# Kernel optimization log

Measured on AMD Instinct MI355X. Metric: run time of the kernel, lower is better.

## Reference

```python
import jax, jax.numpy as jnp
import numpy as np

B, T, D_IN, D_MODEL = 4, 4096, 256, 128


def setup_inputs() -> dict:
    key = jax.random.key(0)
    ks = jax.random.split(key, 7)
    s_in = 1.0 / np.sqrt(D_IN)
    return {
        "x": jax.random.normal(ks[0], (B, T, D_IN), dtype=jnp.float32),
        "Wq": jax.random.normal(ks[1], (D_IN, D_MODEL), dtype=jnp.float32) * s_in,
        "bq": jnp.zeros((D_MODEL,), dtype=jnp.float32),
        "Wk": jax.random.normal(ks[2], (D_IN, D_MODEL), dtype=jnp.float32) * s_in,
        "bk": jnp.zeros((D_MODEL,), dtype=jnp.float32),
        "Wv": jax.random.normal(ks[3], (D_IN, D_MODEL), dtype=jnp.float32) * s_in,
        "bv": jnp.zeros((D_MODEL,), dtype=jnp.float32),
    }


def reference(x, Wq, bq, Wk, bk, Wv, bv):
    # projections: (B,T,d_in) @ (d_in,d_model) -> (B,T,d_model)
    q = x @ Wq + bq
    k = x @ Wk + bk
    v = x @ Wv + bv
    # scores: (B,T,T), scaled by sqrt(d_model)
    scores = jnp.einsum("btd,bsd->bts", q, k) / np.sqrt(D_MODEL).astype(np.float32)
    attn = jax.nn.softmax(scores, axis=-1)
    out = jnp.einsum("bts,bsd->btd", attn, v)
    return out, attn
```

## Files before the change

kernel.cpp:

```cpp
#include <hip/hip_runtime.h>
#include <hip/hip_bf16.h>
#include <stdint.h>

#define TT 4096
#define DM 128
#define DIN 256
#define NB 4

typedef __attribute__((ext_vector_type(4))) float f32x4;
typedef __attribute__((ext_vector_type(8))) short s16x8;
typedef __attribute__((ext_vector_type(4))) short s16x4;

__device__ __forceinline__ unsigned short f2bf(float f) {
    union { float f; unsigned int u; } v; v.f = f;
    return (unsigned short)((v.u + 0x7FFFu + ((v.u >> 16) & 1u)) >> 16);
}
__device__ __forceinline__ float bf2f(unsigned short h) {
    union { unsigned int u; float f; } v; v.u = ((unsigned int)h) << 16;
    return v.f;
}

__global__ __launch_bounds__(256) void k_wt(const float* __restrict__ Wq,
                                            const float* __restrict__ Wk,
                                            const float* __restrict__ Wv,
                                            unsigned short* __restrict__ Wtb) {
    int tid = blockIdx.x * 256 + threadIdx.x;
    int m = tid >> 15;
    int r = tid & 32767;
    int n = r >> 8;
    int k = r & 255;
    const float* W = (m == 0) ? Wq : (m == 1) ? Wk : Wv;
    Wtb[(size_t)tid] = f2bf(W[k * DM + n]);
}

__global__ __launch_bounds__(256) void k_proj(const float* __restrict__ x,
        const float* __restrict__ bq, const float* __restrict__ bk, const float* __restrict__ bv,
        const unsigned short* __restrict__ Wtb,
        unsigned short* __restrict__ Qb, unsigned short* __restrict__ Kb,
        unsigned short* __restrict__ Vb) {
    __shared__ __align__(16) unsigned short wt[DM][40];
    __shared__ __align__(16) unsigned short xl[64][40];
    int m = blockIdx.x >> 8;
    int tile = blockIdx.x & 255;
    int rowbase = tile * 64;
    int i = threadIdx.x;
    int w = i >> 6, l = i & 63;
    int lg = l >> 4, ll = l & 15;
    const float* bias = (m == 0) ? bq : (m == 1) ? bk : bv;
    unsigned short* out = (m == 0) ? Qb : (m == 1) ? Kb : Vb;
    const unsigned short* wsrc = Wtb + (size_t)m * DM * DIN;

    f32x4 acc[8];
    for (int n = 0; n < 8; n++) acc[n] = (f32x4){0.f, 0.f, 0.f, 0.f};

    for (int kk = 0; kk < 8; kk++) {
        int k0 = kk * 32;
        for (int t = 0; t < 2; t++) {
            int idx = i + t * 256;
            int row = idx >> 2, c8 = idx & 3;
            s16x8 v = *(const s16x8*)(wsrc + (size_t)row * DIN + k0 + c8 * 8);
            *(s16x8*)(&wt[row][c8 * 8]) = v;
        }
        for (int t = 0; t < 2; t++) {
            int idx = i + t * 256;
            int row = idx >> 3, c4 = idx & 7;
            f32x4 v = *(const f32x4*)(x + (size_t)(rowbase + row) * DIN + k0 + c4 * 4);
            s16x4 h;
            for (int j = 0; j < 4; j++) h[j] = (short)f2bf(v[j]);
            *(s16x4*)(&xl[row][c4 * 4]) = h;
        }
        __syncthreads();
        s16x8 a = *(const s16x8*)(&xl[w * 16 + ll][lg * 8]);
        for (int n = 0; n < 8; n++) {
            s16x8 b = *(const s16x8*)(&wt[n * 16 + ll][lg * 8]);
            acc[n] = __builtin_amdgcn_mfma_f32_16x16x32_bf16(a, b, acc[n], 0, 0, 0);
        }
        __syncthreads();
    }
    for (int n = 0; n < 8; n++) {
        int col = n * 16 + ll;
        float bv_ = bias[col];
        for (int j = 0; j < 4; j++) {
            int row = rowbase + w * 16 + lg * 4 + j;
            out[(size_t)row * DM + col] = f2bf(acc[n][j] + bv_);
        }
    }
}

__global__ __launch_bounds__(256) void k_vt(const unsigned short* __restrict__ Vb,
                                            unsigned short* __restrict__ Vtb) {
    __shared__ __align__(16) unsigned short tile[64][72];
    int bid = blockIdx.x;
    int b = bid >> 7;
    int rem = bid & 127;
    int tI = rem >> 1, dI = rem & 1;
    int t0 = tI * 64, d0 = dI * 64;
    int i = threadIdx.x;
    for (int t = 0; t < 2; t++) {
        int idx = i + t * 256;
        int r = idx >> 3, c8 = idx & 7;
        s16x8 v = *(const s16x8*)(Vb + ((size_t)(b * TT) + t0 + r) * DM + d0 + c8 * 8);
        *(s16x8*)(&tile[r][c8 * 8]) = v;
    }
    __syncthreads();
    for (int t = 0; t < 2; t++) {
        int idx = i + t * 256;
        int r2 = idx >> 3, c8 = idx & 7;
        s16x8 v;
        for (int j = 0; j < 8; j++) v[j] = (short)tile[c8 * 8 + j][r2];
        *(s16x8*)(Vtb + ((size_t)b * DM + d0 + r2) * TT + t0 + c8 * 8) = v;
    }
}

__global__ __launch_bounds__(512) void k_attn(const unsigned short* __restrict__ Qb,
        const unsigned short* __restrict__ Kb, const unsigned short* __restrict__ Vtb,
        float* __restrict__ outO, float* __restrict__ outA) {
    __shared__ __align__(16) char smem[40448];
    unsigned short* Kl = (unsigned short*)smem;
    unsigned short* Vl = (unsigned short*)(smem + 17408);
    unsigned short* Pl = (unsigned short*)(smem + 35840);

    int bid = blockIdx.x;
    int id2 = (bid & 7) * 64 + (bid >> 3);
    int b = id2 >> 7;
    int rowbase = (id2 & 127) * 32;
    int i = threadIdx.x;
    int w = i >> 6, l = i & 63;
    int rh = w & 1, kh = w >> 1;
    int r2 = w & 1, h2 = (w >> 1) & 1, c2 = w >> 2;
    int lg = l >> 4, ll = l & 15;

    const unsigned short* Qrow = Qb + ((size_t)(b * TT) + rowbase) * DM;
    const unsigned short* Krow = Kb + (size_t)(b * TT) * DM;
    const unsigned short* Vtb_b = Vtb + (size_t)b * DM * TT;
    const float scale = 0.08838834764831845f;

    s16x8 qf[4];
    for (int c = 0; c < 4; c++)
        qf[c] = *(const s16x8*)(Qrow + (size_t)(rh * 16 + ll) * DM + c * 32 + lg * 8);

    float rs[4] = {0.f, 0.f, 0.f, 0.f};
    for (int s0 = 0; s0 < TT; s0 += 64) {
        for (int t = 0; t < 2; t++) {
            int idx = i + t * 512;
            int row = idx >> 4, c8 = idx & 15;
            s16x8 v = *(const s16x8*)(Krow + (size_t)(s0 + row) * DM + c8 * 8);
            *(s16x8*)(&Kl[row * 136 + c8 * 8]) = v;
        }
        __syncthreads();
        {
            f32x4 acc = (f32x4){0.f, 0.f, 0.f, 0.f};
            int kcol = kh * 16 + ll;
            for (int c = 0; c < 4; c++) {
                s16x8 bfr = *(const s16x8*)(&Kl[kcol * 136 + c * 32 + lg * 8]);
                acc = __builtin_amdgcn_mfma_f32_16x16x32_bf16(qf[c], bfr, acc, 0, 0, 0);
            }
            for (int j = 0; j < 4; j++) rs[j] += __expf(acc[j] * scale);
        }
        __syncthreads();
    }
    for (int mm = 1; mm < 16; mm <<= 1)
        for (int j = 0; j < 4; j++) rs[j] += __shfl_xor(rs[j], mm, 64);
    float* rsx = (float*)Pl;
    if (ll == 0)
        for (int j = 0; j < 4; j++) rsx[(kh * 2 + rh) * 16 + lg * 4 + j] = rs[j];
    __syncthreads();
    float inv[4];
    for (int j = 0; j < 4; j++) {
        float tot = rsx[(0 * 2 + rh) * 16 + lg * 4 + j] + rsx[(1 * 2 + rh) * 16 + lg * 4 + j]
                  + rsx[(2 * 2 + rh) * 16 + lg * 4 + j] + rsx[(3 * 2 + rh) * 16 + lg * 4 + j];
        inv[j] = 1.0f / tot;
    }

    f32x4 oacc[4];
    for (int n = 0; n < 4; n++) oacc[n] = (f32x4){0.f, 0.f, 0.f, 0.f};

    for (int s0 = 0; s0 < TT; s0 += 64) {
        for (int t = 0; t < 2; t++) {
            int idx = i + t * 512;
            int row = idx >> 4, c8 = idx & 15;
            s16x8 v = *(const s16x8*)(Krow + (size_t)(s0 + row) * DM + c8 * 8);
            *(s16x8*)(&Kl[row * 136 + c8 * 8]) = v;
        }
        for (int t = 0; t < 2; t++) {
            int idx = i + t * 512;
            int row = idx >> 3, c8 = idx & 7;
            s16x8 v = *(const s16x8*)(Vtb_b + (size_t)row * TT + s0 + c8 * 8);
            *(s16x8*)(&Vl[row * 72 + c8 * 8]) = v;
        }
        __syncthreads();
        {
            f32x4 acc = (f32x4){0.f, 0.f, 0.f, 0.f};
            int kcol = kh * 16 + ll;
            for (int c = 0; c < 4; c++) {
                s16x8 bfr = *(const s16x8*)(&Kl[kcol * 136 + c * 32 + lg * 8]);
                acc = __builtin_amdgcn_mfma_f32_16x16x32_bf16(qf[c], bfr, acc, 0, 0, 0);
            }
            for (int j = 0; j < 4; j++) {
                float p = __expf(acc[j] * scale) * inv[j];
                outA[((size_t)(b * TT) + rowbase + rh * 16 + lg * 4 + j) * TT
                     + s0 + kh * 16 + ll] = p;
                Pl[(rh * 16 + lg * 4 + j) * 72 + kh * 16 + ll] = f2bf(p);
            }
        }
        __syncthreads();
        {
            s16x8 af = *(const s16x8*)(&Pl[(r2 * 16 + ll) * 72 + h2 * 32 + lg * 8]);
            for (int n8 = 0; n8 < 4; n8++) {
                s16x8 bfr = *(const s16x8*)(&Vl[(c2 * 64 + n8 * 16 + ll) * 72 + h2 * 32 + lg * 8]);
                oacc[n8] = __builtin_amdgcn_mfma_f32_16x16x32_bf16(af, bfr, oacc[n8], 0, 0, 0);
            }
        }
        __syncthreads();
    }

    float* Osc = (float*)smem;
    if (h2 == 0) {
        for (int n8 = 0; n8 < 4; n8++)
            for (int j = 0; j < 4; j++) {
                int row = r2 * 16 + lg * 4 + j, col = c2 * 64 + n8 * 16 + ll;
                Osc[row * 132 + col] = oacc[n8][j];
            }
    }
    __syncthreads();
    if (h2 == 1) {
        for (int n8 = 0; n8 < 4; n8++)
            for (int j = 0; j < 4; j++) {
                int row = r2 * 16 + lg * 4 + j, col = c2 * 64 + n8 * 16 + ll;
                float v = oacc[n8][j] + Osc[row * 132 + col];
                outO[((size_t)(b * TT) + rowbase + row) * DM + col] = v;
            }
    }
}

extern "C" void kernel_launch(void* const* d_in, const int* in_sizes, int n_in,
                              void* d_out, int out_size, void* d_ws, size_t ws_size,
                              hipStream_t stream) {
    const float* x  = (const float*)d_in[0];
    const float* Wq = (const float*)d_in[1];
    const float* bq = (const float*)d_in[2];
    const float* Wk = (const float*)d_in[3];
    const float* bk = (const float*)d_in[4];
    const float* Wv = (const float*)d_in[5];
    const float* bv = (const float*)d_in[6];
    float* outO = (float*)d_out;
    float* outA = outO + (size_t)NB * TT * DM;

    char* ws = (char*)d_ws;
    unsigned short* Qb  = (unsigned short*)(ws);
    unsigned short* Kb  = (unsigned short*)(ws + ((size_t)1 << 22));
    unsigned short* Vb  = (unsigned short*)(ws + ((size_t)2 << 22));
    unsigned short* Vtb = (unsigned short*)(ws + ((size_t)3 << 22));
    unsigned short* Wtb = (unsigned short*)(ws + ((size_t)4 << 22));

    k_wt<<<dim3(384), dim3(256), 0, stream>>>(Wq, Wk, Wv, Wtb);
    k_proj<<<dim3(768), dim3(256), 0, stream>>>(x, bq, bk, bv, Wtb, Qb, Kb, Vb);
    k_vt<<<dim3(512), dim3(256), 0, stream>>>(Vb, Vtb);
    k_attn<<<dim3(512), dim3(512), 0, stream>>>(Qb, Kb, Vtb, outO, outA);
}
```

Before: 160.6 us.

## Pipeline K/V tiles into LDS with async direct-to-LDS loads and XOR swizzle

Replaces the synchronous register-staged K and V tile loads in both attention passes with global_load_lds direct-to-LDS copies. The row-sum pass uses a triple-buffered K tile and the output pass a double-buffered K/V tile, so loads for future tiles run while the current tile's MFMAs execute. Synchronisation moves from __syncthreads to explicit vmcnt/lgkmcnt waits plus s_barrier. An XOR swizzle on the source addresses replaces padded LDS rows to avoid bank conflicts. This raises LDS use to about 70 KB per block, which may lower occupancy. The vmcnt counts also depend on the interleaved outA stores being counted in order.

Result: faster. 132.8 us (-17.4%).

```diff
diff --git a/kernel.cpp b/kernel.cpp
--- a/kernel.cpp
+++ b/kernel.cpp
@@ -15,9 +15,11 @@
     union { float f; unsigned int u; } v; v.f = f;
     return (unsigned short)((v.u + 0x7FFFu + ((v.u >> 16) & 1u)) >> 16);
 }
-__device__ __forceinline__ float bf2f(unsigned short h) {
-    union { unsigned int u; float f; } v; v.u = ((unsigned int)h) << 16;
-    return v.f;
+
+__device__ __forceinline__ void cp16(const void* g, void* l) {
+    __builtin_amdgcn_global_load_lds(
+        (__attribute__((address_space(1))) unsigned int*)(size_t)g,
+        (__attribute__((address_space(3))) unsigned int*)l, 16, 0, 0);
 }
 
 __global__ __launch_bounds__(256) void k_wt(const float* __restrict__ Wq,
@@ -115,10 +117,8 @@
 __global__ __launch_bounds__(512) void k_attn(const unsigned short* __restrict__ Qb,
         const unsigned short* __restrict__ Kb, const unsigned short* __restrict__ Vtb,
         float* __restrict__ outO, float* __restrict__ outA) {
-    __shared__ __align__(16) char smem[40448];
-    unsigned short* Kl = (unsigned short*)smem;
-    unsigned short* Vl = (unsigned short*)(smem + 17408);
-    unsigned short* Pl = (unsigned short*)(smem + 35840);
+    __shared__ __align__(16) char smem[70144];
+    unsigned short* Pl = (unsigned short*)(smem + 65536);
 
     int bid = blockIdx.x;
     int id2 = (bid & 7) * 64 + (bid >> 3);
@@ -135,29 +135,57 @@
     const unsigned short* Vtb_b = Vtb + (size_t)b * DM * TT;
     const float scale = 0.08838834764831845f;
 
+    int kch0 = w * 2;
+    int krow_l = l >> 4;
+    int kg_l = l & 15;
+    int vch0 = w * 2;
+    int vrow_l = l >> 3;
+    int vg_l = l & 7;
+
     s16x8 qf[4];
     for (int c = 0; c < 4; c++)
         qf[c] = *(const s16x8*)(Qrow + (size_t)(rh * 16 + ll) * DM + c * 32 + lg * 8);
 
+    int kr = kh * 16 + ll;
+
     float rs[4] = {0.f, 0.f, 0.f, 0.f};
-    for (int s0 = 0; s0 < TT; s0 += 64) {
-        for (int t = 0; t < 2; t++) {
-            int idx = i + t * 512;
-            int row = idx >> 4, c8 = idx & 15;
-            s16x8 v = *(const s16x8*)(Krow + (size_t)(s0 + row) * DM + c8 * 8);
-            *(s16x8*)(&Kl[row * 136 + c8 * 8]) = v;
-        }
-        __syncthreads();
-        {
+    {
+        for (int pt = 0; pt < 2; pt++) {
+            char* kbuf = smem + pt * 16384;
+            for (int t = 0; t < 2; t++) {
+                int ch = kch0 + t;
+                int row = pt * 64 + ch * 4 + krow_l;
+                int g = kg_l ^ (row & 7);
+                cp16(Krow + (size_t)row * DM + g * 8, kbuf + ch * 1024);
+            }
+        }
+        asm volatile("s_waitcnt vmcnt(2)" ::: "memory");
+        __builtin_amdgcn_s_barrier();
+
+        int idx = 0;
+        for (int t = 0; t < 64; t++) {
+            if (t + 2 < 64) {
+                int pidx = idx + 2; if (pidx >= 3) pidx -= 3;
+                char* kbuf = smem + pidx * 16384;
+                int s0n = (t + 2) * 64;
+                for (int u = 0; u < 2; u++) {
+                    int ch = kch0 + u;
+                    int row = ch * 4 + krow_l;
+                    int g = kg_l ^ (row & 7);
+                    cp16(Krow + (size_t)(s0n + row) * DM + g * 8, kbuf + ch * 1024);
+                }
+            }
+            const char* kb = smem + idx * 16384 + kr * 256;
             f32x4 acc = (f32x4){0.f, 0.f, 0.f, 0.f};
-            int kcol = kh * 16 + ll;
             for (int c = 0; c < 4; c++) {
-                s16x8 bfr = *(const s16x8*)(&Kl[kcol * 136 + c * 32 + lg * 8]);
+                s16x8 bfr = *(const s16x8*)(kb + (((c * 4 + lg) ^ (kr & 7)) << 4));
                 acc = __builtin_amdgcn_mfma_f32_16x16x32_bf16(qf[c], bfr, acc, 0, 0, 0);
             }
             for (int j = 0; j < 4; j++) rs[j] += __expf(acc[j] * scale);
-        }
-        __syncthreads();
+            asm volatile("s_waitcnt vmcnt(2)" ::: "memory");
+            __builtin_amdgcn_s_barrier();
+            idx++; if (idx >= 3) idx = 0;
+        }
     }
     for (int mm = 1; mm < 16; mm <<= 1)
         for (int j = 0; j < 4; j++) rs[j] += __shfl_xor(rs[j], mm, 64);
@@ -171,47 +199,75 @@
                   + rsx[(2 * 2 + rh) * 16 + lg * 4 + j] + rsx[(3 * 2 + rh) * 16 + lg * 4 + j];
         inv[j] = 1.0f / tot;
     }
+    __syncthreads();
 
     f32x4 oacc[4];
     for (int n = 0; n < 4; n++) oacc[n] = (f32x4){0.f, 0.f, 0.f, 0.f};
 
-    for (int s0 = 0; s0 < TT; s0 += 64) {
-        for (int t = 0; t < 2; t++) {
-            int idx = i + t * 512;
-            int row = idx >> 4, c8 = idx & 15;
-            s16x8 v = *(const s16x8*)(Krow + (size_t)(s0 + row) * DM + c8 * 8);
-            *(s16x8*)(&Kl[row * 136 + c8 * 8]) = v;
-        }
-        for (int t = 0; t < 2; t++) {
-            int idx = i + t * 512;
-            int row = idx >> 3, c8 = idx & 7;
-            s16x8 v = *(const s16x8*)(Vtb_b + (size_t)row * TT + s0 + c8 * 8);
-            *(s16x8*)(&Vl[row * 72 + c8 * 8]) = v;
-        }
-        __syncthreads();
+    {
+        char* kbuf = smem;
+        char* vbuf = smem + 32768;
+        for (int u = 0; u < 2; u++) {
+            int ch = kch0 + u;
+            int row = ch * 4 + krow_l;
+            int g = kg_l ^ (row & 7);
+            cp16(Krow + (size_t)row * DM + g * 8, kbuf + ch * 1024);
+        }
+        for (int u = 0; u < 2; u++) {
+            int ch = vch0 + u;
+            int row = ch * 8 + vrow_l;
+            int g = vg_l ^ (row & 7);
+            cp16(Vtb_b + (size_t)row * TT + g * 8, vbuf + ch * 1024);
+        }
+    }
+    asm volatile("s_waitcnt vmcnt(0)" ::: "memory");
+    __builtin_amdgcn_s_barrier();
+
+    int cur = 0;
+    for (int t = 0; t < 64; t++) {
+        int s0 = t * 64;
+        if (t < 63) {
+            char* kbuf = smem + (cur ^ 1) * 16384;
+            char* vbuf = smem + 32768 + (cur ^ 1) * 16384;
+            for (int u = 0; u < 2; u++) {
+                int ch = kch0 + u;
+                int row = ch * 4 + krow_l;
+                int g = kg_l ^ (row & 7);
+                cp16(Krow + (size_t)(s0 + 64 + row) * DM + g * 8, kbuf + ch * 1024);
+            }
+            for (int u = 0; u < 2; u++) {
+                int ch = vch0 + u;
+                int row = ch * 8 + vrow_l;
+                int g = vg_l ^ (row & 7);
+                cp16(Vtb_b + (size_t)row * TT + s0 + 64 + g * 8, vbuf + ch * 1024);
+            }
+        }
+        const char* kb = smem + cur * 16384 + kr * 256;
+        f32x4 acc = (f32x4){0.f, 0.f, 0.f, 0.f};
+        for (int c = 0; c < 4; c++) {
+            s16x8 bfr = *(const s16x8*)(kb + (((c * 4 + lg) ^ (kr & 7)) << 4));
+            acc = __builtin_amdgcn_mfma_f32_16x16x32_bf16(qf[c], bfr, acc, 0, 0, 0);
+        }
+        for (int j = 0; j < 4; j++) {
+            float p = __expf(acc[j] * scale) * inv[j];
+            outA[((size_t)(b * TT) + rowbase + rh * 16 + lg * 4 + j) * TT
+                 + s0 + kh * 16 + ll] = p;
+            Pl[(rh * 16 + lg * 4 + j) * 72 + kh * 16 + ll] = f2bf(p);
+        }
+        asm volatile("s_waitcnt lgkmcnt(0)" ::: "memory");
+        __builtin_amdgcn_s_barrier();
         {
-            f32x4 acc = (f32x4){0.f, 0.f, 0.f, 0.f};
-            int kcol = kh * 16 + ll;
-            for (int c = 0; c < 4; c++) {
-                s16x8 bfr = *(const s16x8*)(&Kl[kcol * 136 + c * 32 + lg * 8]);
-                acc = __builtin_amdgcn_mfma_f32_16x16x32_bf16(qf[c], bfr, acc, 0, 0, 0);
-            }
-            for (int j = 0; j < 4; j++) {
-                float p = __expf(acc[j] * scale) * inv[j];
-                outA[((size_t)(b * TT) + rowbase + rh * 16 + lg * 4 + j) * TT
-                     + s0 + kh * 16 + ll] = p;
-                Pl[(rh * 16 + lg * 4 + j) * 72 + kh * 16 + ll] = f2bf(p);
-            }
-        }
-        __syncthreads();
-        {
-            s16x8 af = *(const s16x8*)(&Pl[(r2 * 16 + ll) * 72 + h2 * 32 + lg * 8]);
+            s16x8 af = *(const s16x8*)(Pl + (r2 * 16 + ll) * 72 + h2 * 32 + lg * 8);
+            const char* vb = smem + 32768 + cur * 16384;
             for (int n8 = 0; n8 < 4; n8++) {
-                s16x8 bfr = *(const s16x8*)(&Vl[(c2 * 64 + n8 * 16 + ll) * 72 + h2 * 32 + lg * 8]);
+                int vr = c2 * 64 + n8 * 16 + ll;
+                s16x8 bfr = *(const s16x8*)(vb + vr * 128 + (((h2 * 4 + lg) ^ (vr & 7)) << 4));
                 oacc[n8] = __builtin_amdgcn_mfma_f32_16x16x32_bf16(af, bfr, oacc[n8], 0, 0, 0);
             }
         }
-        __syncthreads();
+        asm volatile("s_waitcnt vmcnt(4)" ::: "memory");
+        __builtin_amdgcn_s_barrier();
+        cur ^= 1;
     }
 
     float* Osc = (float*)smem;
```

## Split key range across warps with direct global fragment loads in attention

Applied to the files above, without the earlier changes.

The attention kernel now uses 4 waves per block, and each wave owns a contiguous quarter of the key sequence. Each wave loads K and V^T MFMA fragments straight from global memory rather than staging them through shared LDS tiles, so the per-tile __syncthreads barriers go away. Partial row sums and partial output accumulators are reduced across waves at the end through shared memory. This removes block-wide synchronization and the cooperative LDS copies, but it raises register pressure (two 16x128 output accumulator sets per wave) and relies on cache hits for K/V loads that have no coalescing-friendly staging.

After: 226.9 us. 41.2% more time.

```diff
diff --git a/kernel.cpp b/kernel.cpp
--- a/kernel.cpp
+++ b/kernel.cpp
@@ -14,10 +14,6 @@
 __device__ __forceinline__ unsigned short f2bf(float f) {
     union { float f; unsigned int u; } v; v.f = f;
     return (unsigned short)((v.u + 0x7FFFu + ((v.u >> 16) & 1u)) >> 16);
-}
-__device__ __forceinline__ float bf2f(unsigned short h) {
-    union { unsigned int u; float f; } v; v.u = ((unsigned int)h) << 16;
-    return v.f;
 }
 
 __global__ __launch_bounds__(256) void k_wt(const float* __restrict__ Wq,
@@ -112,13 +108,10 @@
     }
 }
 
-__global__ __launch_bounds__(512) void k_attn(const unsigned short* __restrict__ Qb,
+__global__ __launch_bounds__(256, 2) void k_attn(const unsigned short* __restrict__ Qb,
         const unsigned short* __restrict__ Kb, const unsigned short* __restrict__ Vtb,
         float* __restrict__ outO, float* __restrict__ outA) {
-    __shared__ __align__(16) char smem[40448];
-    unsigned short* Kl = (unsigned short*)smem;
-    unsigned short* Vl = (unsigned short*)(smem + 17408);
-    unsigned short* Pl = (unsigned short*)(smem + 35840);
+    __shared__ __align__(16) char smem[44544];
 
     int bid = blockIdx.x;
     int id2 = (bid & 7) * 64 + (bid >> 3);
@@ -126,110 +119,120 @@
     int rowbase = (id2 & 127) * 32;
     int i = threadIdx.x;
     int w = i >> 6, l = i & 63;
-    int rh = w & 1, kh = w >> 1;
-    int r2 = w & 1, h2 = (w >> 1) & 1, c2 = w >> 2;
     int lg = l >> 4, ll = l & 15;
 
     const unsigned short* Qrow = Qb + ((size_t)(b * TT) + rowbase) * DM;
     const unsigned short* Krow = Kb + (size_t)(b * TT) * DM;
-    const unsigned short* Vtb_b = Vtb + (size_t)b * DM * TT;
+    const unsigned short* Vt_b = Vtb + (size_t)b * DM * TT;
     const float scale = 0.08838834764831845f;
 
-    s16x8 qf[4];
-    for (int c = 0; c < 4; c++)
-        qf[c] = *(const s16x8*)(Qrow + (size_t)(rh * 16 + ll) * DM + c * 32 + lg * 8);
-
-    float rs[4] = {0.f, 0.f, 0.f, 0.f};
-    for (int s0 = 0; s0 < TT; s0 += 64) {
-        for (int t = 0; t < 2; t++) {
-            int idx = i + t * 512;
-            int row = idx >> 4, c8 = idx & 15;
-            s16x8 v = *(const s16x8*)(Krow + (size_t)(s0 + row) * DM + c8 * 8);
-            *(s16x8*)(&Kl[row * 136 + c8 * 8]) = v;
-        }
-        __syncthreads();
-        {
-            f32x4 acc = (f32x4){0.f, 0.f, 0.f, 0.f};
-            int kcol = kh * 16 + ll;
+    s16x8 qf[2][4];
+    for (int rh = 0; rh < 2; rh++)
+        for (int c = 0; c < 4; c++)
+            qf[rh][c] = *(const s16x8*)(Qrow + (size_t)(rh * 16 + ll) * DM + c * 32 + lg * 8);
+
+    float rs[2][4] = {{0.f,0.f,0.f,0.f},{0.f,0.f,0.f,0.f}};
+    for (int cc = 0; cc < 32; cc++) {
+        int s0 = w * 1024 + cc * 32;
+        for (int kh = 0; kh < 2; kh++) {
+            s16x8 kf[4];
+            for (int c = 0; c < 4; c++)
+                kf[c] = *(const s16x8*)(Krow + (size_t)(s0 + kh * 16 + ll) * DM + c * 32 + lg * 8);
+            f32x4 a0 = (f32x4){0.f,0.f,0.f,0.f}, a1 = (f32x4){0.f,0.f,0.f,0.f};
             for (int c = 0; c < 4; c++) {
-                s16x8 bfr = *(const s16x8*)(&Kl[kcol * 136 + c * 32 + lg * 8]);
-                acc = __builtin_amdgcn_mfma_f32_16x16x32_bf16(qf[c], bfr, acc, 0, 0, 0);
-            }
-            for (int j = 0; j < 4; j++) rs[j] += __expf(acc[j] * scale);
-        }
-        __syncthreads();
+                a0 = __builtin_amdgcn_mfma_f32_16x16x32_bf16(qf[0][c], kf[c], a0, 0, 0, 0);
+                a1 = __builtin_amdgcn_mfma_f32_16x16x32_bf16(qf[1][c], kf[c], a1, 0, 0, 0);
+            }
+            for (int j = 0; j < 4; j++) {
+                rs[0][j] += __expf(a0[j] * scale);
+                rs[1][j] += __expf(a1[j] * scale);
+            }
+        }
     }
     for (int mm = 1; mm < 16; mm <<= 1)
-        for (int j = 0; j < 4; j++) rs[j] += __shfl_xor(rs[j], mm, 64);
-    float* rsx = (float*)Pl;
+        for (int rh = 0; rh < 2; rh++)
+            for (int j = 0; j < 4; j++)
+                rs[rh][j] += __shfl_xor(rs[rh][j], mm, 64);
+    float* rsx = (float*)(smem + 10240);
     if (ll == 0)
-        for (int j = 0; j < 4; j++) rsx[(kh * 2 + rh) * 16 + lg * 4 + j] = rs[j];
-    __syncthreads();
-    float inv[4];
-    for (int j = 0; j < 4; j++) {
-        float tot = rsx[(0 * 2 + rh) * 16 + lg * 4 + j] + rsx[(1 * 2 + rh) * 16 + lg * 4 + j]
-                  + rsx[(2 * 2 + rh) * 16 + lg * 4 + j] + rsx[(3 * 2 + rh) * 16 + lg * 4 + j];
-        inv[j] = 1.0f / tot;
-    }
-
-    f32x4 oacc[4];
-    for (int n = 0; n < 4; n++) oacc[n] = (f32x4){0.f, 0.f, 0.f, 0.f};
-
-    for (int s0 = 0; s0 < TT; s0 += 64) {
-        for (int t = 0; t < 2; t++) {
-            int idx = i + t * 512;
-            int row = idx >> 4, c8 = idx & 15;
-            s16x8 v = *(const s16x8*)(Krow + (size_t)(s0 + row) * DM + c8 * 8);
-            *(s16x8*)(&Kl[row * 136 + c8 * 8]) = v;
-        }
-        for (int t = 0; t < 2; t++) {
-            int idx = i + t * 512;
-            int row = idx >> 3, c8 = idx & 7;
-            s16x8 v = *(const s16x8*)(Vtb_b + (size_t)row * TT + s0 + c8 * 8);
-            *(s16x8*)(&Vl[row * 72 + c8 * 8]) = v;
-        }
-        __syncthreads();
-        {
-            f32x4 acc = (f32x4){0.f, 0.f, 0.f, 0.f};
-            int kcol = kh * 16 + ll;
+        for (int rh = 0; rh < 2; rh++)
+            for (int j = 0; j < 4; j++)
+                rsx[w * 32 + rh * 16 + lg * 4 + j] = rs[rh][j];
+    __syncthreads();
+    float inv[2][4];
+    for (int rh = 0; rh < 2; rh++)
+        for (int j = 0; j < 4; j++) {
+            int row = rh * 16 + lg * 4 + j;
+            inv[rh][j] = 1.0f / (rsx[row] + rsx[32 + row] + rsx[64 + row] + rsx[96 + row]);
+        }
+
+    f32x4 oacc[2][8];
+    for (int rh = 0; rh < 2; rh++)
+        for (int n = 0; n < 8; n++)
+            oacc[rh][n] = (f32x4){0.f,0.f,0.f,0.f};
+    unsigned short* Pw = (unsigned short*)(smem + w * 2560);
+
+    for (int cc = 0; cc < 32; cc++) {
+        int s0 = w * 1024 + cc * 32;
+        for (int kh = 0; kh < 2; kh++) {
+            s16x8 kf[4];
+            for (int c = 0; c < 4; c++)
+                kf[c] = *(const s16x8*)(Krow + (size_t)(s0 + kh * 16 + ll) * DM + c * 32 + lg * 8);
+            f32x4 a0 = (f32x4){0.f,0.f,0.f,0.f}, a1 = (f32x4){0.f,0.f,0.f,0.f};
             for (int c = 0; c < 4; c++) {
-                s16x8 bfr = *(const s16x8*)(&Kl[kcol * 136 + c * 32 + lg * 8]);
-                acc = __builtin_amdgcn_mfma_f32_16x16x32_bf16(qf[c], bfr, acc, 0, 0, 0);
+                a0 = __builtin_amdgcn_mfma_f32_16x16x32_bf16(qf[0][c], kf[c], a0, 0, 0, 0);
+                a1 = __builtin_amdgcn_mfma_f32_16x16x32_bf16(qf[1][c], kf[c], a1, 0, 0, 0);
             }
             for (int j = 0; j < 4; j++) {
-                float p = __expf(acc[j] * scale) * inv[j];
-                outA[((size_t)(b * TT) + rowbase + rh * 16 + lg * 4 + j) * TT
-                     + s0 + kh * 16 + ll] = p;
-                Pl[(rh * 16 + lg * 4 + j) * 72 + kh * 16 + ll] = f2bf(p);
-            }
-        }
-        __syncthreads();
-        {
-            s16x8 af = *(const s16x8*)(&Pl[(r2 * 16 + ll) * 72 + h2 * 32 + lg * 8]);
-            for (int n8 = 0; n8 < 4; n8++) {
-                s16x8 bfr = *(const s16x8*)(&Vl[(c2 * 64 + n8 * 16 + ll) * 72 + h2 * 32 + lg * 8]);
-                oacc[n8] = __builtin_amdgcn_mfma_f32_16x16x32_bf16(af, bfr, oacc[n8], 0, 0, 0);
-            }
-        }
-        __syncthreads();
-    }
-
-    float* Osc = (float*)smem;
-    if (h2 == 0) {
-        for (int n8 = 0; n8 < 4; n8++)
-            for (int j = 0; j < 4; j++) {
-                int row = r2 * 16 + lg * 4 + j, col = c2 * 64 + n8 * 16 + ll;
-                Osc[row * 132 + col] = oacc[n8][j];
-            }
-    }
-    __syncthreads();
-    if (h2 == 1) {
-        for (int n8 = 0; n8 < 4; n8++)
-            for (int j = 0; j < 4; j++) {
-                int row = r2 * 16 + lg * 4 + j, col = c2 * 64 + n8 * 16 + ll;
-                float v = oacc[n8][j] + Osc[row * 132 + col];
-                outO[((size_t)(b * TT) + rowbase + row) * DM + col] = v;
-            }
+                float p0 = __expf(a0[j] * scale) * inv[0][j];
+                float p1 = __expf(a1[j] * scale) * inv[1][j];
+                outA[((size_t)(b * TT) + rowbase + lg * 4 + j) * TT + s0 + kh * 16 + ll] = p0;
+                outA[((size_t)(b * TT) + rowbase + 16 + lg * 4 + j) * TT + s0 + kh * 16 + ll] = p1;
+                Pw[(lg * 4 + j) * 40 + kh * 16 + ll] = f2bf(p0);
+                Pw[(16 + lg * 4 + j) * 40 + kh * 16 + ll] = f2bf(p1);
+            }
+        }
+        s16x8 pa0 = *(const s16x8*)(Pw + (size_t)ll * 40 + lg * 8);
+        s16x8 pa1 = *(const s16x8*)(Pw + (size_t)(16 + ll) * 40 + lg * 8);
+        for (int n = 0; n < 8; n++) {
+            s16x8 vf = *(const s16x8*)(Vt_b + (size_t)(n * 16 + ll) * TT + s0 + lg * 8);
+            oacc[0][n] = __builtin_amdgcn_mfma_f32_16x16x32_bf16(pa0, vf, oacc[0][n], 0, 0, 0);
+            oacc[1][n] = __builtin_amdgcn_mfma_f32_16x16x32_bf16(pa1, vf, oacc[1][n], 0, 0, 0);
+        }
+    }
+
+    float* obuf = (float*)(smem + 10752);
+    if (w >= 2) {
+        float* dst = obuf + (size_t)(w - 2) * 32 * 132;
+        for (int rh = 0; rh < 2; rh++)
+            for (int n = 0; n < 8; n++)
+                for (int j = 0; j < 4; j++)
+                    dst[(rh * 16 + lg * 4 + j) * 132 + n * 16 + ll] = oacc[rh][n][j];
+    }
+    __syncthreads();
+    if (w < 2) {
+        float* src = obuf + (size_t)w * 32 * 132;
+        for (int rh = 0; rh < 2; rh++)
+            for (int n = 0; n < 8; n++)
+                for (int j = 0; j < 4; j++)
+                    oacc[rh][n][j] += src[(rh * 16 + lg * 4 + j) * 132 + n * 16 + ll];
+        if (w == 1) {
+            for (int rh = 0; rh < 2; rh++)
+                for (int n = 0; n < 8; n++)
+                    for (int j = 0; j < 4; j++)
+                        src[(rh * 16 + lg * 4 + j) * 132 + n * 16 + ll] = oacc[rh][n][j];
+        }
+    }
+    __syncthreads();
+    if (w == 0) {
+        float* src = obuf + (size_t)1 * 32 * 132;
+        for (int rh = 0; rh < 2; rh++)
+            for (int n = 0; n < 8; n++)
+                for (int j = 0; j < 4; j++) {
+                    int row = rh * 16 + lg * 4 + j, col = n * 16 + ll;
+                    float v = oacc[rh][n][j] + src[row * 132 + col];
+                    outO[((size_t)(b * TT) + rowbase + row) * DM + col] = v;
+                }
     }
 }
 
@@ -256,5 +259,5 @@
     k_wt<<<dim3(384), dim3(256), 0, stream>>>(Wq, Wk, Wv, Wtb);
     k_proj<<<dim3(768), dim3(256), 0, stream>>>(x, bq, bk, bv, Wtb, Qb, Kb, Vb);
     k_vt<<<dim3(512), dim3(256), 0, stream>>>(Vb, Vtb);
-    k_attn<<<dim3(512), dim3(512), 0, stream>>>(Qb, Kb, Vtb, outO, outA);
-}
+    k_attn<<<dim3(512), dim3(256), 0, stream>>>(Qb, Kb, Vtb, outO, outA);
+}
```

## Pipeline K/V staging with async global-to-LDS copies and per-wave P buffers

Applied to the files above, without the earlier changes.

Replaces register-staged K/V tile loads with direct global-to-LDS asynchronous copies into XOR-swizzled multi-buffered tiles. The row-sum pass uses a 4-deep ring, and the output pass double-buffers K and V, so loads overlap MFMA work and fewer full barriers are needed. Each wave now keeps its own P tile, zero-padded to the 32-wide MFMA K dimension. That avoids a cross-wave barrier but doubles the PV MFMA count. Attention probabilities are written as 16-byte vector stores, read back from the bf16 P tile, so outA now carries bf16-rounded values, a precision risk.

After: 147.6 us. 8.1% less time.

```diff
diff --git a/kernel.cpp b/kernel.cpp
--- a/kernel.cpp
+++ b/kernel.cpp
@@ -18,6 +18,12 @@
 __device__ __forceinline__ float bf2f(unsigned short h) {
     union { unsigned int u; float f; } v; v.u = ((unsigned int)h) << 16;
     return v.f;
+}
+
+__device__ __forceinline__ void cp16(const void* g, void* l) {
+    __builtin_amdgcn_global_load_lds(
+        (__attribute__((address_space(1))) unsigned int*)(size_t)g,
+        (__attribute__((address_space(3))) unsigned int*)l, 16, 0, 0);
 }
 
 __global__ __launch_bounds__(256) void k_wt(const float* __restrict__ Wq,
@@ -112,13 +118,10 @@
     }
 }
 
-__global__ __launch_bounds__(512) void k_attn(const unsigned short* __restrict__ Qb,
+__global__ __launch_bounds__(512, 4) void k_attn(const unsigned short* __restrict__ Qb,
         const unsigned short* __restrict__ Kb, const unsigned short* __restrict__ Vtb,
         float* __restrict__ outO, float* __restrict__ outA) {
-    __shared__ __align__(16) char smem[40448];
-    unsigned short* Kl = (unsigned short*)smem;
-    unsigned short* Vl = (unsigned short*)(smem + 17408);
-    unsigned short* Pl = (unsigned short*)(smem + 35840);
+    __shared__ __align__(16) char smem[76288];
 
     int bid = blockIdx.x;
     int id2 = (bid & 7) * 64 + (bid >> 3);
@@ -126,110 +129,147 @@
     int rowbase = (id2 & 127) * 32;
     int i = threadIdx.x;
     int w = i >> 6, l = i & 63;
-    int rh = w & 1, kh = w >> 1;
-    int r2 = w & 1, h2 = (w >> 1) & 1, c2 = w >> 2;
+    int rg = w & 1, ks = w >> 1;
     int lg = l >> 4, ll = l & 15;
 
     const unsigned short* Qrow = Qb + ((size_t)(b * TT) + rowbase) * DM;
     const unsigned short* Krow = Kb + (size_t)(b * TT) * DM;
-    const unsigned short* Vtb_b = Vtb + (size_t)b * DM * TT;
+    const unsigned short* Vt_b = Vtb + (size_t)b * DM * TT;
     const float scale = 0.08838834764831845f;
+
+    unsigned short* Pw = (unsigned short*)(smem + 65536 + w * 1280);
+    float* rsx = (float*)(smem + 75776);
 
     s16x8 qf[4];
     for (int c = 0; c < 4; c++)
-        qf[c] = *(const s16x8*)(Qrow + (size_t)(rh * 16 + ll) * DM + c * 32 + lg * 8);
+        qf[c] = *(const s16x8*)(Qrow + (size_t)(rg * 16 + ll) * DM + c * 32 + lg * 8);
+
+    int kr = ks * 16 + ll;
+
+    auto stage_k = [&](char* kbuf, int s0) {
+        for (int u = 0; u < 2; u++) {
+            int c = u * 8 + w;
+            int row = c * 4 + (l >> 4);
+            int g = (l & 15) ^ (row & 7);
+            cp16(Krow + (size_t)(s0 + row) * DM + g * 8, kbuf + c * 1024);
+        }
+    };
+    auto stage_v = [&](char* vbuf, int s0) {
+        for (int u = 0; u < 2; u++) {
+            int c = u * 8 + w;
+            int row = c * 8 + (l >> 3);
+            int g = (l & 7) ^ (row & 7);
+            cp16(Vt_b + (size_t)row * TT + s0 + g * 8, vbuf + c * 1024);
+        }
+    };
+    auto qk = [&](const char* kbuf) -> f32x4 {
+        const char* kbase = kbuf + kr * 256;
+        f32x4 acc = (f32x4){0.f, 0.f, 0.f, 0.f};
+        for (int c = 0; c < 4; c++) {
+            s16x8 kf = *(const s16x8*)(kbase + (((c * 4 + lg) ^ (kr & 7)) << 4));
+            acc = __builtin_amdgcn_mfma_f32_16x16x32_bf16(qf[c], kf, acc, 0, 0, 0);
+        }
+        return acc;
+    };
 
     float rs[4] = {0.f, 0.f, 0.f, 0.f};
-    for (int s0 = 0; s0 < TT; s0 += 64) {
-        for (int t = 0; t < 2; t++) {
-            int idx = i + t * 512;
-            int row = idx >> 4, c8 = idx & 15;
-            s16x8 v = *(const s16x8*)(Krow + (size_t)(s0 + row) * DM + c8 * 8);
-            *(s16x8*)(&Kl[row * 136 + c8 * 8]) = v;
-        }
-        __syncthreads();
-        {
-            f32x4 acc = (f32x4){0.f, 0.f, 0.f, 0.f};
-            int kcol = kh * 16 + ll;
-            for (int c = 0; c < 4; c++) {
-                s16x8 bfr = *(const s16x8*)(&Kl[kcol * 136 + c * 32 + lg * 8]);
-                acc = __builtin_amdgcn_mfma_f32_16x16x32_bf16(qf[c], bfr, acc, 0, 0, 0);
-            }
-            for (int j = 0; j < 4; j++) rs[j] += __expf(acc[j] * scale);
-        }
-        __syncthreads();
-    }
+    stage_k(smem, 0);
+    stage_k(smem + 16384, 64);
+    stage_k(smem + 32768, 128);
+    asm volatile("s_waitcnt vmcnt(4)" ::: "memory");
+    __builtin_amdgcn_s_barrier();
+    for (int t = 0; t < 64; t++) {
+        if (t + 3 < 64) stage_k(smem + ((t + 3) & 3) * 16384, (t + 3) * 64);
+        f32x4 acc = qk(smem + (t & 3) * 16384);
+        for (int j = 0; j < 4; j++) rs[j] += __expf(acc[j] * scale);
+        asm volatile("s_waitcnt vmcnt(4)" ::: "memory");
+        __builtin_amdgcn_s_barrier();
+    }
+    asm volatile("s_waitcnt vmcnt(0)" ::: "memory");
+
     for (int mm = 1; mm < 16; mm <<= 1)
         for (int j = 0; j < 4; j++) rs[j] += __shfl_xor(rs[j], mm, 64);
-    float* rsx = (float*)Pl;
     if (ll == 0)
-        for (int j = 0; j < 4; j++) rsx[(kh * 2 + rh) * 16 + lg * 4 + j] = rs[j];
+        for (int j = 0; j < 4; j++) rsx[ks * 32 + rg * 16 + lg * 4 + j] = rs[j];
     __syncthreads();
-    float inv[4];
+    float inv_[4];
     for (int j = 0; j < 4; j++) {
-        float tot = rsx[(0 * 2 + rh) * 16 + lg * 4 + j] + rsx[(1 * 2 + rh) * 16 + lg * 4 + j]
-                  + rsx[(2 * 2 + rh) * 16 + lg * 4 + j] + rsx[(3 * 2 + rh) * 16 + lg * 4 + j];
-        inv[j] = 1.0f / tot;
-    }
-
-    f32x4 oacc[4];
-    for (int n = 0; n < 4; n++) oacc[n] = (f32x4){0.f, 0.f, 0.f, 0.f};
-
-    for (int s0 = 0; s0 < TT; s0 += 64) {
-        for (int t = 0; t < 2; t++) {
-            int idx = i + t * 512;
-            int row = idx >> 4, c8 = idx & 15;
-            s16x8 v = *(const s16x8*)(Krow + (size_t)(s0 + row) * DM + c8 * 8);
-            *(s16x8*)(&Kl[row * 136 + c8 * 8]) = v;
-        }
-        for (int t = 0; t < 2; t++) {
-            int idx = i + t * 512;
-            int row = idx >> 3, c8 = idx & 7;
-            s16x8 v = *(const s16x8*)(Vtb_b + (size_t)row * TT + s0 + c8 * 8);
-            *(s16x8*)(&Vl[row * 72 + c8 * 8]) = v;
-        }
-        __syncthreads();
+        int row = rg * 16 + lg * 4 + j;
+        inv_[j] = 1.0f / (rsx[row] + rsx[32 + row] + rsx[64 + row] + rsx[96 + row]);
+    }
+
+    for (int j = 0; j < 4; j++) Pw[(lg * 4 + j) * 40 + 16 + ll] = 0;
+    f32x4 oacc[8];
+    for (int n = 0; n < 8; n++) oacc[n] = (f32x4){0.f, 0.f, 0.f, 0.f};
+
+    stage_k(smem, 0);
+    stage_v(smem + 32768, 0);
+    asm volatile("s_waitcnt vmcnt(0)" ::: "memory");
+    __builtin_amdgcn_s_barrier();
+
+    int cur = 0;
+    for (int t = 0; t < 64; t++) {
+        int s0 = t * 64;
+        if (t < 63) {
+            stage_k(smem + (cur ^ 1) * 16384, s0 + 64);
+            stage_v(smem + 32768 + (cur ^ 1) * 16384, s0 + 64);
+        }
+        f32x4 acc = qk(smem + cur * 16384);
+        for (int j = 0; j < 4; j++) {
+            float p = __expf(acc[j] * scale) * inv_[j];
+            Pw[(lg * 4 + j) * 40 + ll] = f2bf(p);
+        }
+        asm volatile("s_waitcnt lgkmcnt(0)" ::: "memory");
+        __builtin_amdgcn_sched_barrier(0);
+        s16x8 paf = *(const s16x8*)(Pw + ll * 40 + lg * 8);
+        const char* vbuf = smem + 32768 + cur * 16384;
+        for (int n8 = 0; n8 < 8; n8++) {
+            int row = n8 * 16 + ll;
+            int gl = ks * 2 + (lg & 1);
+            s16x8 bfr = *(const s16x8*)(vbuf + row * 128 + ((gl ^ (row & 7)) << 4));
+            oacc[n8] = __builtin_amdgcn_mfma_f32_16x16x32_bf16(paf, bfr, oacc[n8], 0, 0, 0);
+        }
         {
-            f32x4 acc = (f32x4){0.f, 0.f, 0.f, 0.f};
-            int kcol = kh * 16 + ll;
-            for (int c = 0; c < 4; c++) {
-                s16x8 bfr = *(const s16x8*)(&Kl[kcol * 136 + c * 32 + lg * 8]);
-                acc = __builtin_amdgcn_mfma_f32_16x16x32_bf16(qf[c], bfr, acc, 0, 0, 0);
+            int arow = l >> 2, acol = (l & 3) * 4;
+            s16x4 pv = *(const s16x4*)(Pw + arow * 40 + acol);
+            f32x4 fv;
+            for (int q = 0; q < 4; q++) fv[q] = bf2f((unsigned short)pv[q]);
+            *(f32x4*)(outA + ((size_t)(b * TT) + rowbase + rg * 16 + arow) * TT
+                      + s0 + ks * 16 + acol) = fv;
+        }
+        asm volatile("s_waitcnt vmcnt(1)" ::: "memory");
+        __builtin_amdgcn_s_barrier();
+        cur ^= 1;
+    }
+
+    float* obuf = (float*)smem;
+    if (ks >= 1) {
+        float* dst = obuf + (size_t)(rg * 3 + ks - 1) * 2112;
+        for (int n8 = 0; n8 < 8; n8++)
+            for (int j = 0; j < 4; j++)
+                dst[(lg * 4 + j) * 132 + n8 * 16 + ll] = oacc[n8][j];
+    }
+    __syncthreads();
+    if (ks == 0) {
+        float* s1 = obuf + (size_t)(rg * 3 + 0) * 2112;
+        float* s2 = obuf + (size_t)(rg * 3 + 1) * 2112;
+        float* s3 = obuf + (size_t)(rg * 3 + 2) * 2112;
+        for (int n8 = 0; n8 < 8; n8++)
+            for (int j = 0; j < 4; j++) {
+                int idx = (lg * 4 + j) * 132 + n8 * 16 + ll;
+                s1[idx] = oacc[n8][j] + s1[idx] + s2[idx] + s3[idx];
             }
-            for (int j = 0; j < 4; j++) {
-                float p = __expf(acc[j] * scale) * inv[j];
-                outA[((size_t)(b * TT) + rowbase + rh * 16 + lg * 4 + j) * TT
-                     + s0 + kh * 16 + ll] = p;
-                Pl[(rh * 16 + lg * 4 + j) * 72 + kh * 16 + ll] = f2bf(p);
-            }
-        }
-        __syncthreads();
-        {
-            s16x8 af = *(const s16x8*)(&Pl[(r2 * 16 + ll) * 72 + h2 * 32 + lg * 8]);
-            for (int n8 = 0; n8 < 4; n8++) {
-                s16x8 bfr = *(const s16x8*)(&Vl[(c2 * 64 + n8 * 16 + ll) * 72 + h2 * 32 + lg * 8]);
-                oacc[n8] = __builtin_amdgcn_mfma_f32_16x16x32_bf16(af, bfr, oacc[n8], 0, 0, 0);
-            }
-        }
-        __syncthreads();
-    }
-
-    float* Osc = (float*)smem;
-    if (h2 == 0) {
-        for (int n8 = 0; n8 < 4; n8++)
-            for (int j = 0; j < 4; j++) {
-                int row = r2 * 16 + lg * 4 + j, col = c2 * 64 + n8 * 16 + ll;
-                Osc[row * 132 + col] = oacc[n8][j];
-            }
     }
     __syncthreads();
-    if (h2 == 1) {
-        for (int n8 = 0; n8 < 4; n8++)
-            for (int j = 0; j < 4; j++) {
-                int row = r2 * 16 + lg * 4 + j, col = c2 * 64 + n8 * 16 + ll;
-                float v = oacc[n8][j] + Osc[row * 132 + col];
-                outO[((size_t)(b * TT) + rowbase + row) * DM + col] = v;
-            }
+    {
+        int row = i >> 4;
+        int col = (i & 15) * 8;
+        const float* src = obuf + (size_t)((row >> 4) * 3) * 2112 + (row & 15) * 132 + col;
+        f32x4 v0 = *(const f32x4*)(src);
+        f32x4 v1 = *(const f32x4*)(src + 4);
+        float* dst = outO + ((size_t)(b * TT) + rowbase + row) * DM + col;
+        *(f32x4*)dst = v0;
+        *(f32x4*)(dst + 4) = v1;
     }
 }
 
```
